# Optimization experiments

Measured on AMD Instinct MI355X. Metric: run time of the kernel, lower is better.

## Reference

```python
import jax, jax.numpy as jnp
import numpy as np

N_TOKEN = 8192
N_EMBED = 512
N_SAMPLE = 10
TAU = 1.0
RHO = 1.0


def setup_inputs() -> dict:
    key = jax.random.key(0)
    k1, k2 = jax.random.split(key)
    inputs = jax.random.normal(k1, (4, 2048, N_EMBED), dtype=jnp.float32)
    embeds = jax.random.normal(k2, (N_TOKEN, N_EMBED), dtype=jnp.float32)
    return {"inputs": inputs, "embeds": embeds}


def reference(inputs, embeds):
    size = inputs.shape
    x = inputs.reshape(-1, N_EMBED)  # (N, D)
    n = x.shape[0]
    # squared distances, scaled by n_token (as in get_distances)
    dists = (jnp.sum(x * x, axis=-1, keepdims=True)
             + jnp.sum(embeds * embeds, axis=-1)[None, :]
             - 2.0 * jnp.matmul(x, embeds.T)) / N_TOKEN  # (N, K)
    logits = -dists / TAU  # categorical(softmax(logits)) == categorical(logits)
    skey = jax.random.fold_in(jax.random.key(0), 1)
    # multinomial with replacement: n_sample i.i.d. categorical draws per row
    samples = jax.random.categorical(skey, logits[:, None, :], axis=-1,
                                     shape=(n, N_SAMPLE))  # (N, n_sample) int
    quantized_embs = embeds[samples].mean(axis=1)  # (N, D) gather + mean
    quantized = x + jax.lax.stop_gradient(quantized_embs - x)  # straight-through
    gkey = jax.random.fold_in(jax.random.key(0), 2)
    gates = jax.random.bernoulli(gkey, RHO, (n,)).astype(x.dtype)[:, None]
    quantized = quantized * gates + (1.0 - gates) * x
    quantized = quantized.reshape(size)
    samples = samples.reshape(size[:-1] + (N_SAMPLE,))
    return quantized, samples
```

## Files before the change

kernel.cpp:

```cpp
#include <hip/hip_runtime.h>
#include <stdint.h>
#include <math.h>

#define N_ROWS 8192
#define N_TOK  8192
#define N_DIM  512
#define N_SAMP 10
#define GK     1536

typedef __attribute__((ext_vector_type(8))) short bf16x8_t;
typedef __attribute__((ext_vector_type(4))) float f32x4_t;

__host__ __device__ __forceinline__ void tf2x32(uint32_t ks0, uint32_t ks1,
                                                uint32_t& x0, uint32_t& x1) {
  uint32_t ks2 = ks0 ^ ks1 ^ 0x1BD11BDAu;
  x0 += ks0; x1 += ks1;
#define TF_ROUND(r) { x0 += x1; x1 = __builtin_rotateleft32(x1, r); x1 ^= x0; }
  TF_ROUND(13) TF_ROUND(15) TF_ROUND(26) TF_ROUND(6)
  x0 += ks1; x1 += ks2 + 1u;
  TF_ROUND(17) TF_ROUND(29) TF_ROUND(16) TF_ROUND(24)
  x0 += ks2; x1 += ks0 + 2u;
  TF_ROUND(13) TF_ROUND(15) TF_ROUND(26) TF_ROUND(6)
  x0 += ks0; x1 += ks1 + 3u;
  TF_ROUND(17) TF_ROUND(29) TF_ROUND(16) TF_ROUND(24)
  x0 += ks1; x1 += ks2 + 4u;
  TF_ROUND(13) TF_ROUND(15) TF_ROUND(26) TF_ROUND(6)
  x0 += ks2; x1 += ks0 + 5u;
#undef TF_ROUND
}

__device__ __forceinline__ unsigned short f2bf_rne(float f) {
  uint32_t u = __float_as_uint(f);
  uint32_t r = (u + 0x7fffu + ((u >> 16) & 1u)) >> 16;
  return (unsigned short)r;
}
__device__ __forceinline__ float bf2f(unsigned short h) {
  return __uint_as_float((uint32_t)h << 16);
}

__device__ __forceinline__ unsigned long long shfl_xor_u64(unsigned long long v, int off) {
  uint32_t lo = (uint32_t)v, hi = (uint32_t)(v >> 32);
  lo = (uint32_t)__shfl_xor((int)lo, off, 64);
  hi = (uint32_t)__shfl_xor((int)hi, off, 64);
  return ((unsigned long long)hi << 32) | lo;
}

__global__ __launch_bounds__(256) void rownorm_kernel(const float* __restrict__ M,
                                                      float* __restrict__ out) {
  int lane = threadIdx.x & 63;
  int row = (int)((blockIdx.x * blockDim.x + threadIdx.x) >> 6);
  const float* p = M + (size_t)row * N_DIM;
  float acc = 0.f;
#pragma unroll
  for (int d = 0; d < N_DIM; d += 64) {
    float v = p[d + lane];
    acc = fmaf(v, v, acc);
  }
#pragma unroll
  for (int off = 32; off; off >>= 1) acc += __shfl_xor(acc, off, 64);
  if (lane == 0) out[row] = acc;
}

__global__ __launch_bounds__(256) void init_champ_kernel(unsigned long long* __restrict__ c) {
  int i = blockIdx.x * 256 + threadIdx.x;
  if (i < N_ROWS * N_SAMP) c[i] = 0xFFFFFFFFFFFFFFFFULL;
}

__global__ __launch_bounds__(256) void init_state_kernel(float* __restrict__ rmin,
                                                         int* __restrict__ ridx) {
  int i = blockIdx.x * 256 + threadIdx.x;
  if (i < N_ROWS * N_SAMP) { rmin[i] = INFINITY; ridx[i] = 0; }
}

__global__ __launch_bounds__(256) void split_kernel(const float* __restrict__ src,
                                                    unsigned short* __restrict__ dst,
                                                    int mode) {
  int t = blockIdx.x * 256 + threadIdx.x;
  int row = t >> 7;
  int c = (t & 127) << 2;
  float4 v = *(const float4*)(src + (size_t)row * N_DIM + c);
  ushort4 hi, lo;
  hi.x = f2bf_rne(v.x); lo.x = f2bf_rne(v.x - bf2f(hi.x));
  hi.y = f2bf_rne(v.y); lo.y = f2bf_rne(v.y - bf2f(hi.y));
  hi.z = f2bf_rne(v.z); lo.z = f2bf_rne(v.z - bf2f(hi.z));
  hi.w = f2bf_rne(v.w); lo.w = f2bf_rne(v.w - bf2f(hi.w));
  unsigned short* base = dst + (size_t)row * GK;
  *(ushort4*)(base + c) = hi;
  if (mode == 0) {
    *(ushort4*)(base + 512 + c) = lo;
    *(ushort4*)(base + 1024 + c) = hi;
  } else {
    *(ushort4*)(base + 512 + c) = hi;
    *(ushort4*)(base + 1024 + c) = lo;
  }
}

__device__ __forceinline__ void async_cp16(const void* g, void* l) {
  __builtin_amdgcn_global_load_lds((const __attribute__((address_space(1))) void*)g,
                                   (__attribute__((address_space(3))) void*)l, 16, 0, 0);
}

__global__ __launch_bounds__(256) void fused_gemm_sample_kernel(
    const unsigned short* __restrict__ A2, const unsigned short* __restrict__ B2,
    const float* __restrict__ xx, const float* __restrict__ ee,
    unsigned long long* __restrict__ champ, uint32_t k0, uint32_t k1) {
  __shared__ __align__(16) unsigned char smem[65536];
  unsigned short* As = (unsigned short*)smem;
  unsigned short* Bs = (unsigned short*)(smem + 16384);
  float* Et = (float*)smem;
  int tid = threadIdx.x;
  int w = tid >> 6, l = tid & 63;

  int bid = blockIdx.y * gridDim.x + blockIdx.x;
  int by = bid & 63;
  int bx = bid >> 6;

  int row0 = by * 128;
  int col0 = bx * 128;
  int wm = (w & 1) * 64, wn = (w >> 1) * 64;
  int quad = l >> 4, r15 = l & 15;

  f32x4_t acc[4][4];
#pragma unroll
  for (int i = 0; i < 4; ++i)
#pragma unroll
    for (int j = 0; j < 4; ++j) acc[i][j] = (f32x4_t){0.f, 0.f, 0.f, 0.f};

  int srow[4], skc[4];
#pragma unroll
  for (int r = 0; r < 4; ++r) {
    int c = tid + 256 * r;
    srow[r] = c >> 3;
    skc[r] = (c & 7) ^ (srow[r] & 7);
  }

  for (int kt = 0; kt < GK; kt += 64) {
#pragma unroll
    for (int r = 0; r < 4; ++r) {
      int c = tid + 256 * r;
      async_cp16(A2 + (size_t)(row0 + srow[r]) * GK + kt + skc[r] * 8, As + c * 8);
      async_cp16(B2 + (size_t)(col0 + srow[r]) * GK + kt + skc[r] * 8, Bs + c * 8);
    }
    __syncthreads();

#pragma unroll
    for (int kk2 = 0; kk2 < 2; ++kk2) {
      bf16x8_t af[4], bf[4];
#pragma unroll
      for (int i = 0; i < 4; ++i) {
        int row = wm + i * 16 + r15;
        int qc = (kk2 * 4 + quad) ^ (r15 & 7);
        af[i] = *(const bf16x8_t*)&As[row * 64 + qc * 8];
      }
#pragma unroll
      for (int j = 0; j < 4; ++j) {
        int row = wn + j * 16 + r15;
        int qc = (kk2 * 4 + quad) ^ (r15 & 7);
        bf[j] = *(const bf16x8_t*)&Bs[row * 64 + qc * 8];
      }
#pragma unroll
      for (int i = 0; i < 4; ++i)
#pragma unroll
        for (int j = 0; j < 4; ++j)
          acc[i][j] = __builtin_amdgcn_mfma_f32_16x16x32_bf16(af[i], bf[j], acc[i][j], 0, 0, 0);
    }
    __syncthreads();
  }

  const float inv_nt = 1.f / 8192.f;
  float eev[4];
#pragma unroll
  for (int j = 0; j < 4; ++j) eev[j] = ee[col0 + wn + j * 16 + r15];
#pragma unroll
  for (int i = 0; i < 4; ++i) {
#pragma unroll
    for (int r = 0; r < 4; ++r) {
      int lrow = wm + i * 16 + quad * 4 + r;
      float xxv = xx[row0 + lrow];
      int mxr = lrow & 31;
#pragma unroll
      for (int j = 0; j < 4; ++j) {
        int col = wn + j * 16 + r15;
        float dist = (xxv + eev[j] - 2.0f * acc[i][j][r]) * inv_nt;
        Et[lrow * 128 + (col ^ mxr)] = expf(dist);
      }
    }
  }
  __syncthreads();

  int lrow = tid >> 1, half = tid & 1;
  int grow = row0 + lrow;
  unsigned long long* cg = champ + (size_t)grow * N_SAMP;
  unsigned long long cw[N_SAMP];
  uint32_t th[N_SAMP];
  int improved = 0;
#pragma unroll
  for (int s = 0; s < N_SAMP; ++s) {
    unsigned long long c = cg[s];
    cw[s] = 0xFFFFFFFFFFFFFFFFULL;
    uint32_t hi = (uint32_t)(c >> 32);
    uint32_t t = 0u;
    if (hi < 0x7F800000u) {
      float ut = expf(-__uint_as_float(hi)) * 0.999999f;
      t = ((uint32_t)(ut * 8388608.0f)) << 9;
    }
    th[s] = t;
  }
  const float tiny = 1.1754943508222875e-38f;
  uint32_t row_c = (uint32_t)grow * 81920u;
  const float* Erow = Et + lrow * 128 + half * 64;
  int mxr = lrow & 31;
  uint32_t kbase = (uint32_t)(col0 + half * 64);

  for (int kk = 0; kk < 64; ++kk) {
    uint32_t base_c = row_c + kbase + (uint32_t)kk;
#pragma unroll
    for (int s = 0; s < N_SAMP; ++s) {
      uint32_t x0 = 0u, x1 = base_c + (uint32_t)s * 8192u;
      tf2x32(k0, k1, x0, x1);
      uint32_t bits = x0 ^ x1;
      bool cand = (bits >= th[s]);
      if (__any(cand)) {
        if (cand) {
          float Ek = Erow[kk ^ mxr];
          float u = __uint_as_float(0x3f800000u | (bits >> 9)) - 1.0f;
          u = fmaxf(u, tiny);
          float wv = -logf(u) * Ek;
          unsigned long long p = ((unsigned long long)__float_as_uint(wv) << 32)
                               | (kbase + (uint32_t)kk);
          if (p < cw[s]) {
            cw[s] = p;
            float ut = expf(-wv) * 0.999999f;
            uint32_t nt = ((uint32_t)(ut * 8388608.0f)) << 9;
            th[s] = (nt > th[s]) ? nt : th[s];
            improved |= (1 << s);
          }
        }
      }
    }
  }
#pragma unroll
  for (int s = 0; s < N_SAMP; ++s)
    if (improved & (1 << s)) atomicMin(&cg[s], cw[s]);
}

__global__ __launch_bounds__(256) void gemm_nt_kernel(const float* __restrict__ A,
                                                      const float* __restrict__ B,
                                                      const float* __restrict__ xx,
                                                      const float* __restrict__ ee,
                                                      float* __restrict__ E,
                                                      int ks, int KC) {
  __shared__ __align__(16) float Asf[32][68];
  __shared__ __align__(16) float Bsf[32][68];
  int tid = threadIdx.x;
  int row0 = blockIdx.y * 64;
  int colB0 = blockIdx.x * 64 + ks;
  int tx = tid & 15, ty = tid >> 4;
  float acc[4][4] = {};
  for (int d0 = 0; d0 < N_DIM; d0 += 32) {
#pragma unroll
    for (int r = 0; r < 2; ++r) {
      int c = tid + 256 * r;
      int m = c >> 3;
      int dv = (c & 7) << 2;
      const float4 va = *(const float4*)(A + (size_t)(row0 + m) * N_DIM + d0 + dv);
      Asf[dv + 0][m] = va.x; Asf[dv + 1][m] = va.y;
      Asf[dv + 2][m] = va.z; Asf[dv + 3][m] = va.w;
      const float4 vb = *(const float4*)(B + (size_t)(colB0 + m) * N_DIM + d0 + dv);
      Bsf[dv + 0][m] = vb.x; Bsf[dv + 1][m] = vb.y;
      Bsf[dv + 2][m] = vb.z; Bsf[dv + 3][m] = vb.w;
    }
    __syncthreads();
#pragma unroll
    for (int dd = 0; dd < 32; ++dd) {
      float4 a4 = *(const float4*)&Asf[dd][ty << 2];
      float4 b4 = *(const float4*)&Bsf[dd][tx << 2];
      float av[4] = {a4.x, a4.y, a4.z, a4.w};
      float bv[4] = {b4.x, b4.y, b4.z, b4.w};
#pragma unroll
      for (int i = 0; i < 4; ++i)
#pragma unroll
        for (int j = 0; j < 4; ++j)
          acc[i][j] = fmaf(av[i], bv[j], acc[i][j]);
    }
    __syncthreads();
  }
  const float inv_nt = 1.f / 8192.f;
  int colC0 = blockIdx.x * 64;
  float eev[4];
#pragma unroll
  for (int j = 0; j < 4; ++j) eev[j] = ee[ks + colC0 + (tx << 2) + j];
#pragma unroll
  for (int i = 0; i < 4; ++i) {
    int grow = row0 + (ty << 2) + i;
    float xxv = xx[grow];
    float4 v;
    v.x = expf((xxv + eev[0] - 2.0f * acc[i][0]) * inv_nt);
    v.y = expf((xxv + eev[1] - 2.0f * acc[i][1]) * inv_nt);
    v.z = expf((xxv + eev[2] - 2.0f * acc[i][2]) * inv_nt);
    v.w = expf((xxv + eev[3] - 2.0f * acc[i][3]) * inv_nt);
    *(float4*)(E + (size_t)grow * KC + colC0 + (tx << 2)) = v;
  }
}

__global__ __launch_bounds__(256) void sample_kernel(const float* __restrict__ E,
                                                     float* __restrict__ rmin,
                                                     int* __restrict__ ridx,
                                                     int ks, int KC,
                                                     uint32_t k0, uint32_t k1) {
  int lane = threadIdx.x & 63;
  int row = (int)((blockIdx.x * blockDim.x + threadIdx.x) >> 6);
  unsigned long long champ[N_SAMP];
  uint32_t th[N_SAMP];
#pragma unroll
  for (int s = 0; s < N_SAMP; ++s) { champ[s] = 0xFFFFFFFFFFFFFFFFULL; th[s] = 0u; }
  const float tiny = 1.1754943508222875e-38f;
  uint32_t row_c = (uint32_t)row * 81920u;
  const float* Erow = E + (size_t)row * KC;

  float Ek = Erow[lane];
  for (int kk = lane; kk < KC; kk += 64) {
    int nk = (kk + 64 < KC) ? kk + 64 : kk;
    float Ekn = Erow[nk];
    uint32_t k = (uint32_t)(ks + kk);
    uint32_t base_c = row_c + k;
#pragma unroll
    for (int s = 0; s < N_SAMP; ++s) {
      uint32_t x0 = 0u, x1 = base_c + (uint32_t)s * 8192u;
      tf2x32(k0, k1, x0, x1);
      uint32_t bits = x0 ^ x1;
      bool cand = (bits >= th[s]);
      if (__any(cand)) {
        float u = __uint_as_float(0x3f800000u | (bits >> 9)) - 1.0f;
        u = fmaxf(u, tiny);
        float wv = -logf(u) * Ek;
        unsigned long long p = cand
            ? (((unsigned long long)__float_as_uint(wv) << 32) | k)
            : 0xFFFFFFFFFFFFFFFFULL;
#pragma unroll
        for (int off = 1; off < 64; off <<= 1) {
          unsigned long long op = shfl_xor_u64(p, off);
          p = (op < p) ? op : p;
        }
        if (p < champ[s]) {
          champ[s] = p;
          float wmin = __uint_as_float((uint32_t)(p >> 32));
          float ut = expf(-wmin) * 0.999999f;
          th[s] = ((uint32_t)(ut * 8388608.0f)) << 9;
        }
      }
    }
    Ek = Ekn;
  }
#pragma unroll
  for (int s = 0; s < N_SAMP; ++s) {
    if (lane == 0) {
      float v = __uint_as_float((uint32_t)(champ[s] >> 32));
      int id = (int)(uint32_t)(champ[s] & 0xFFFFFFFFu);
      size_t p = (size_t)row * N_SAMP + s;
      if (v < rmin[p]) { rmin[p] = v; ridx[p] = id; }
    }
  }
}

__global__ __launch_bounds__(256) void gather_kernel(const float* __restrict__ emb,
                                                     const unsigned long long* __restrict__ champ,
                                                     const float* __restrict__ x,
                                                     float* __restrict__ outq,
                                                     float* __restrict__ outs) {
  int lane = threadIdx.x & 63;
  int row = (int)((blockIdx.x * blockDim.x + threadIdx.x) >> 6);
  int idx[N_SAMP];
#pragma unroll
  for (int s = 0; s < N_SAMP; ++s)
    idx[s] = (int)(uint32_t)(champ[(size_t)row * N_SAMP + s] & 0xFFFFFFFFu);
  if (lane < N_SAMP) outs[row * N_SAMP + lane] = (float)idx[lane];
#pragma unroll
  for (int h = 0; h < 2; ++h) {
    int c = h * 256 + lane * 4;
    float4 sum = make_float4(0.f, 0.f, 0.f, 0.f);
#pragma unroll
    for (int s = 0; s < N_SAMP; ++s) {
      float4 e = *(const float4*)(emb + (size_t)idx[s] * N_DIM + c);
      sum.x += e.x; sum.y += e.y; sum.z += e.z; sum.w += e.w;
    }
    float4 xv = *(const float4*)(x + (size_t)row * N_DIM + c);
    float4 o;
    o.x = xv.x + (sum.x / 10.0f - xv.x);
    o.y = xv.y + (sum.y / 10.0f - xv.y);
    o.z = xv.z + (sum.z / 10.0f - xv.z);
    o.w = xv.w + (sum.w / 10.0f - xv.w);
    *(float4*)(outq + (size_t)row * N_DIM + c) = o;
  }
}

__global__ __launch_bounds__(256) void gather_fb_kernel(const float* __restrict__ emb,
                                                        const int* __restrict__ ridx,
                                                        const float* __restrict__ x,
                                                        float* __restrict__ outq,
                                                        float* __restrict__ outs) {
  int lane = threadIdx.x & 63;
  int row = (int)((blockIdx.x * blockDim.x + threadIdx.x) >> 6);
  int idx[N_SAMP];
#pragma unroll
  for (int s = 0; s < N_SAMP; ++s) idx[s] = ridx[row * N_SAMP + s];
  if (lane < N_SAMP) outs[row * N_SAMP + lane] = (float)idx[lane];
#pragma unroll
  for (int h = 0; h < 2; ++h) {
    int c = h * 256 + lane * 4;
    float4 sum = make_float4(0.f, 0.f, 0.f, 0.f);
#pragma unroll
    for (int s = 0; s < N_SAMP; ++s) {
      float4 e = *(const float4*)(emb + (size_t)idx[s] * N_DIM + c);
      sum.x += e.x; sum.y += e.y; sum.z += e.z; sum.w += e.w;
    }
    float4 xv = *(const float4*)(x + (size_t)row * N_DIM + c);
    float4 o;
    o.x = xv.x + (sum.x / 10.0f - xv.x);
    o.y = xv.y + (sum.y / 10.0f - xv.y);
    o.z = xv.z + (sum.z / 10.0f - xv.z);
    o.w = xv.w + (sum.w / 10.0f - xv.w);
    *(float4*)(outq + (size_t)row * N_DIM + c) = o;
  }
}

extern "C" void kernel_launch(void* const* d_in, const int* in_sizes, int n_in,
                              void* d_out, int out_size, void* d_ws, size_t ws_size,
                              hipStream_t stream) {
  const float* x = (const float*)d_in[0];
  const float* emb = (const float*)d_in[1];
  float* out_q = (float*)d_out;
  float* out_s = out_q + (size_t)N_ROWS * N_DIM;

  const size_t split_u = (size_t)N_ROWS * GK;
  const size_t fixed_f = (size_t)N_ROWS + N_TOK + 2 * (size_t)N_ROWS * N_SAMP;
  const size_t out_f = (size_t)N_ROWS * N_DIM + (size_t)N_ROWS * N_SAMP;

  uint32_t s0 = 0u, s1 = 1u;
  tf2x32(0u, 0u, s0, s1);

  {
    size_t need = (size_t)(N_ROWS + N_TOK) * 4
                + (size_t)N_ROWS * N_SAMP * 8
                + 2 * split_u * 2;
    if (need <= ws_size) {
      float* xx = (float*)d_ws;
      float* ee = xx + N_ROWS;
      unsigned long long* champ = (unsigned long long*)(ee + N_TOK);
      unsigned short* A2 = (unsigned short*)(champ + (size_t)N_ROWS * N_SAMP);
      unsigned short* B2 = A2 + split_u;

      rownorm_kernel<<<2048, 256, 0, stream>>>(x, xx);
      rownorm_kernel<<<2048, 256, 0, stream>>>(emb, ee);
      init_champ_kernel<<<(N_ROWS * N_SAMP + 255) / 256, 256, 0, stream>>>(champ);
      split_kernel<<<N_ROWS * 128 / 256, 256, 0, stream>>>(x, A2, 0);
      split_kernel<<<N_ROWS * 128 / 256, 256, 0, stream>>>(emb, B2, 1);
      fused_gemm_sample_kernel<<<dim3(64, 64), 256, 0, stream>>>(
          A2, B2, xx, ee, champ, s0, s1);
      gather_kernel<<<2048, 256, 0, stream>>>(emb, champ, x, out_q, out_s);
      return;
    }
  }

  float *xx, *ee, *rmin, *E;
  int* ridx;
  int KC = 0;
  for (int c = 8192; c >= 64; c >>= 1) {
    if ((fixed_f + (size_t)N_ROWS * c) * 4 <= ws_size) { KC = c; break; }
  }
  if (KC) {
    xx = (float*)d_ws;
    ee = xx + N_ROWS;
    rmin = ee + N_TOK;
    ridx = (int*)(rmin + (size_t)N_ROWS * N_SAMP);
    E = (float*)(ridx + (size_t)N_ROWS * N_SAMP);
  } else if (fixed_f * 4 <= ws_size) {
    KC = 512;
    xx = (float*)d_ws;
    ee = xx + N_ROWS;
    rmin = ee + N_TOK;
    ridx = (int*)(rmin + (size_t)N_ROWS * N_SAMP);
    E = out_q;
  } else {
    KC = 256;
    E = out_q;
    float* tail = out_q + (out_f - fixed_f);
    xx = tail;
    ee = xx + N_ROWS;
    rmin = ee + N_TOK;
    ridx = (int*)(rmin + (size_t)N_ROWS * N_SAMP);
  }

  rownorm_kernel<<<2048, 256, 0, stream>>>(x, xx);
  rownorm_kernel<<<2048, 256, 0, stream>>>(emb, ee);
  init_state_kernel<<<(N_ROWS * N_SAMP + 255) / 256, 256, 0, stream>>>(rmin, ridx);
  for (int ks = 0; ks < N_TOK; ks += KC) {
    gemm_nt_kernel<<<dim3(KC / 64, N_ROWS / 64), 256, 0, stream>>>(x, emb, xx, ee, E, ks, KC);
    sample_kernel<<<2048, 256, 0, stream>>>(E, rmin, ridx, ks, KC, s0, s1);
  }
  gather_fb_kernel<<<2048, 256, 0, stream>>>(emb, ridx, x, out_q, out_s);
}
```

Measured before the change: 1.546 ms.

## Remap sampling so each wavefront handles one row's columns across lanes

The Gumbel/exponential-race sampling phase is reorganized. Previously each thread owned half a row and walked 64 columns serially. Now each wavefront iterates over 32 rows, with lanes spanning 128 columns in two halves. Candidate minima are reduced across the wave using 64-bit xor shuffles, the next row's champion values are prefetched, and only lane 0 issues the atomicMin calls. This aims to cut divergence, since thresholds become wave-uniform, and to reduce atomics, at the cost of shuffle reductions whenever any lane is a candidate.

```diff
diff --git a/kernel.cpp b/kernel.cpp
--- a/kernel.cpp
+++ b/kernel.cpp
@@ -188,49 +188,68 @@
   }
   __syncthreads();
 
-  int lrow = tid >> 1, half = tid & 1;
-  int grow = row0 + lrow;
-  unsigned long long* cg = champ + (size_t)grow * N_SAMP;
-  unsigned long long cw[N_SAMP];
-  uint32_t th[N_SAMP];
-  int improved = 0;
-#pragma unroll
-  for (int s = 0; s < N_SAMP; ++s) {
-    unsigned long long c = cg[s];
-    cw[s] = 0xFFFFFFFFFFFFFFFFULL;
-    uint32_t hi = (uint32_t)(c >> 32);
-    uint32_t t = 0u;
-    if (hi < 0x7F800000u) {
-      float ut = expf(-__uint_as_float(hi)) * 0.999999f;
-      t = ((uint32_t)(ut * 8388608.0f)) << 9;
-    }
-    th[s] = t;
-  }
   const float tiny = 1.1754943508222875e-38f;
-  uint32_t row_c = (uint32_t)grow * 81920u;
-  const float* Erow = Et + lrow * 128 + half * 64;
-  int mxr = lrow & 31;
-  uint32_t kbase = (uint32_t)(col0 + half * 64);
-
-  for (int kk = 0; kk < 64; ++kk) {
-    uint32_t base_c = row_c + kbase + (uint32_t)kk;
+  int rbeg = w * 32;
+  unsigned long long snap[N_SAMP];
+  {
+    const unsigned long long* cg0 = champ + (size_t)(row0 + rbeg) * N_SAMP;
+#pragma unroll
+    for (int s = 0; s < N_SAMP; ++s) snap[s] = cg0[s];
+  }
+  for (int r = 0; r < 32; ++r) {
+    int lrow = rbeg + r;
+    int grow = row0 + lrow;
+    uint32_t th[N_SAMP];
+    unsigned long long cw[N_SAMP];
+    int improved = 0;
 #pragma unroll
     for (int s = 0; s < N_SAMP; ++s) {
-      uint32_t x0 = 0u, x1 = base_c + (uint32_t)s * 8192u;
-      tf2x32(k0, k1, x0, x1);
-      uint32_t bits = x0 ^ x1;
-      bool cand = (bits >= th[s]);
-      if (__any(cand)) {
-        if (cand) {
-          float Ek = Erow[kk ^ mxr];
+      uint32_t hi = (uint32_t)(snap[s] >> 32);
+      uint32_t t = 0u;
+      if (hi < 0x7F800000u) {
+        float ut = expf(-__uint_as_float(hi)) * 0.999999f;
+        t = ((uint32_t)(ut * 8388608.0f)) << 9;
+      }
+      th[s] = t;
+      cw[s] = 0xFFFFFFFFFFFFFFFFULL;
+    }
+    if (r < 31) {
+      const unsigned long long* cgn = champ + (size_t)(grow + 1) * N_SAMP;
+#pragma unroll
+      for (int s = 0; s < N_SAMP; ++s) snap[s] = cgn[s];
+    }
+    uint32_t row_c = (uint32_t)grow * 81920u;
+    int mxr = lrow & 31;
+    const float* Erow = Et + lrow * 128;
+#pragma unroll
+    for (int half = 0; half < 2; ++half) {
+      int col = half * 64 + l;
+      float Ek = Erow[col ^ mxr];
+      uint32_t kglob = (uint32_t)(col0 + col);
+      uint32_t base_c = row_c + kglob;
+#pragma unroll
+      for (int s = 0; s < N_SAMP; ++s) {
+        uint32_t x0 = 0u, x1 = base_c + (uint32_t)s * 8192u;
+        tf2x32(k0, k1, x0, x1);
+        uint32_t bits = x0 ^ x1;
+        bool cand = (bits >= th[s]);
+        if (__any(cand)) {
+          asm volatile("");
           float u = __uint_as_float(0x3f800000u | (bits >> 9)) - 1.0f;
           u = fmaxf(u, tiny);
           float wv = -logf(u) * Ek;
-          unsigned long long p = ((unsigned long long)__float_as_uint(wv) << 32)
-                               | (kbase + (uint32_t)kk);
+          unsigned long long p = cand
+              ? (((unsigned long long)__float_as_uint(wv) << 32) | kglob)
+              : 0xFFFFFFFFFFFFFFFFULL;
+#pragma unroll
+          for (int off = 1; off < 64; off <<= 1) {
+            unsigned long long op = shfl_xor_u64(p, off);
+            p = (op < p) ? op : p;
+          }
           if (p < cw[s]) {
             cw[s] = p;
-            float ut = expf(-wv) * 0.999999f;
+            float wmin = __uint_as_float((uint32_t)(p >> 32));
+            float ut = expf(-wmin) * 0.999999f;
             uint32_t nt = ((uint32_t)(ut * 8388608.0f)) << 9;
             th[s] = (nt > th[s]) ? nt : th[s];
             improved |= (1 << s);
@@ -238,10 +257,15 @@
         }
       }
     }
-  }
-#pragma unroll
-  for (int s = 0; s < N_SAMP; ++s)
-    if (improved & (1 << s)) atomicMin(&cg[s], cw[s]);
+    if (improved) {
+      if (l == 0) {
+        unsigned long long* cg = champ + (size_t)grow * N_SAMP;
+#pragma unroll
+        for (int s = 0; s < N_SAMP; ++s)
+          if (improved & (1 << s)) atomicMin(&cg[s], cw[s]);
+      }
+    }
+  }
 }
 
 __global__ __launch_bounds__(256) void gemm_nt_kernel(const float* __restrict__ A,
```

New measurement: 1.835 ms. +18.7%, slower.
